# Performance work log

Measured on AMD Instinct MI355X. Metric: run time of the kernel, lower is better.

The kernel has to match this reference:

```python
import jax, jax.numpy as jnp
import numpy as np

B, N, E, L, G, F, H = 64, 500, 16000, 64, 64, 8, 128

def setup_inputs() -> dict:
    key = jax.random.key(0)
    ks = jax.random.split(key, 8)
    return {
        "x": jax.random.normal(ks[0], (B, N, L), dtype=jnp.float32),
        "incidence": jax.random.normal(ks[1], (N, E), dtype=jnp.float32),
        "ef": jax.random.normal(ks[2], (E, F), dtype=jnp.float32),
        "W1": jax.random.normal(ks[3], (F, H), dtype=jnp.float32) * 0.1,
        "b1": jax.random.normal(ks[4], (H,), dtype=jnp.float32) * 0.1,
        "W2": jax.random.normal(ks[5], (H, L * G), dtype=jnp.float32) * 0.1,
        "b2": jax.random.normal(ks[6], (L * G,), dtype=jnp.float32) * 0.1,
        "b_gc": jax.random.normal(ks[7], (G,), dtype=jnp.float32) * 0.1,
    }

def reference(x, incidence, ef, W1, b1, W2, b2, b_gc):
    # MLP-generated per-edge kernel: [E, G, L]
    h = jax.nn.relu(ef @ W1 + b1)
    kernel = (h @ W2 + b2).reshape(E, G, L)
    # gather node features onto edges: [B, E, L]
    t = jnp.einsum('bnl,ne->bel', x, incidence)
    # per-edge batched matvec: [B, E, G]
    y = jnp.einsum('egl,bel->beg', kernel, t)
    # scatter back to nodes: [B, N, G]
    y = jnp.einsum('ne,beg->bng', incidence, y)
    # gc is a frozen identity Linear -> just add bias, then ReLU
    y = jax.nn.relu(y + b_gc)
    return y.reshape(x.shape[0], -1)
```

## Files before the change

kernel.cpp:

```cpp
#include <hip/hip_runtime.h>

constexpr int B_ = 64, N_ = 500, E_ = 16000, L_ = 64, G_ = 64, F_ = 8, H_ = 128;
constexpr int GL_ = 4096;
constexpr int NP_ = 512;
constexpr int KS_ = 4;
constexpr int ACC_ELEMS = B_ * N_ * G_;

using bf16x8  = __attribute__((ext_vector_type(8))) short;
using f32x4   = __attribute__((ext_vector_type(4))) float;
using ushort8 = __attribute__((ext_vector_type(8))) unsigned short;

#define MFMA16(a, b, c) __builtin_amdgcn_mfma_f32_16x16x32_bf16((a), (b), (c), 0, 0, 0)

typedef __attribute__((address_space(3))) unsigned int       lds_u32;
typedef const __attribute__((address_space(1))) unsigned int glb_u32;

static __device__ __forceinline__ unsigned short f2bf(float f) {
    union { float f; unsigned u; } v; v.f = f;
    unsigned r = v.u + 0x7fffu + ((v.u >> 16) & 1u);
    return (unsigned short)(r >> 16);
}
static __device__ __forceinline__ float bf2f(unsigned short s) {
    union { float f; unsigned u; } v; v.u = ((unsigned)s) << 16;
    return v.f;
}

static __device__ __forceinline__ void stage_tile(
    const unsigned short* __restrict__ g, int ld, int r0, int kk,
    unsigned short* lds, int tid)
{
    #pragma unroll
    for (int c = 0; c < 4; ++c) {
        const int ch  = tid + c * 256;
        const int row = ch >> 3;
        const int csw = (ch & 7) ^ (row & 7);
        __builtin_amdgcn_global_load_lds(
            (glb_u32*)(g + (size_t)(r0 + row) * ld + kk + csw * 8),
            (lds_u32*)(lds + (size_t)ch * 8), 16, 0, 0);
    }
}

static __device__ __forceinline__ void gemm_body(
    const unsigned short* __restrict__ A, int lda,
    const unsigned short* __restrict__ Bm, int ldb,
    int K, int nN,
    unsigned short* __restrict__ C, int ldc,
    const float* __restrict__ bias)
{
    const int nwg = gridDim.x;
    const int bid = blockIdx.x;
    const int swz = (nwg & 7) ? bid : ((bid & 7) * (nwg >> 3) + (bid >> 3));
    const int m0 = (swz / nN) * 128, n0 = (swz % nN) * 128;

    const int tid  = threadIdx.x;
    const int lane = tid & 63, wid = tid >> 6;
    const int wm = wid >> 1, wn = wid & 1;
    const int fr = lane & 15, fq = lane >> 4;

    __shared__ __align__(16) unsigned short smem[2 * 128 * 64];
    unsigned short* As = smem;
    unsigned short* Bs = smem + 128 * 64;

    const f32x4 fz = {0.f, 0.f, 0.f, 0.f};
    f32x4 acc[4][4] = {{fz, fz, fz, fz}, {fz, fz, fz, fz},
                       {fz, fz, fz, fz}, {fz, fz, fz, fz}};

    const int rowA[4] = {wm * 64 + 0 * 16 + fr, wm * 64 + 1 * 16 + fr,
                         wm * 64 + 2 * 16 + fr, wm * 64 + 3 * 16 + fr};
    const int rowB[4] = {wn * 64 + 0 * 16 + fr, wn * 64 + 1 * 16 + fr,
                         wn * 64 + 2 * 16 + fr, wn * 64 + 3 * 16 + fr};

    const int nk = K / 64;
    for (int kt = 0; kt < nk; ++kt) {
        stage_tile(A, lda, m0, kt * 64, As, tid);
        stage_tile(Bm, ldb, n0, kt * 64, Bs, tid);
        __syncthreads();
        #pragma unroll
        for (int ks = 0; ks < 2; ++ks) {
            bf16x8 af[4], bf[4];
            #pragma unroll
            for (int i = 0; i < 4; ++i)
                af[i] = *(const bf16x8*)&As[rowA[i] * 64 +
                         (((ks * 4 + fq) ^ (rowA[i] & 7)) * 8)];
            #pragma unroll
            for (int j = 0; j < 4; ++j)
                bf[j] = *(const bf16x8*)&Bs[rowB[j] * 64 +
                         (((ks * 4 + fq) ^ (rowB[j] & 7)) * 8)];
            #pragma unroll
            for (int i = 0; i < 4; ++i)
                #pragma unroll
                for (int j = 0; j < 4; ++j)
                    acc[i][j] = MFMA16(af[i], bf[j], acc[i][j]);
        }
        __syncthreads();
    }

    auto Cs = (unsigned short(*)[128])smem;
    #pragma unroll
    for (int i = 0; i < 4; ++i)
        #pragma unroll
        for (int j = 0; j < 4; ++j) {
            const float bv = bias ? bias[n0 + wn * 64 + j * 16 + fr] : 0.f;
            #pragma unroll
            for (int r = 0; r < 4; ++r)
                Cs[wm * 64 + i * 16 + fq * 4 + r][wn * 64 + j * 16 + fr] =
                    f2bf(acc[i][j][r] + bv);
        }
    __syncthreads();
    const int r2 = tid >> 4, o2 = (tid & 15) * 8;
    #pragma unroll
    for (int i = 0; i < 8; ++i) {
        const int row = i * 16 + r2;
        *(uint4*)&C[(size_t)(m0 + row) * ldc + n0 + o2] = *(const uint4*)&Cs[row][o2];
    }
}

__global__ __launch_bounds__(256)
void gemm_pair(const unsigned short* __restrict__ A0, int lda0,
               const unsigned short* __restrict__ B0, int ldb0, int K0,
               unsigned short* __restrict__ C0, const float* __restrict__ bias0,
               const unsigned short* __restrict__ A1, int lda1,
               const unsigned short* __restrict__ B1, int ldb1, int K1,
               unsigned short* __restrict__ C1, int nN)
{
    if (blockIdx.y == 0)
        gemm_body(A0, lda0, B0, ldb0, K0, nN, C0, GL_, bias0);
    else
        gemm_body(A1, lda1, B1, ldb1, K1, nN, C1, GL_, nullptr);
}

__global__ __launch_bounds__(512)
void k_y8(unsigned short* tc, const unsigned short* __restrict__ Kc)
{
    const int e0 = blockIdx.x * 8;
    const int tid = threadIdx.x, lane = tid & 63, w = tid >> 6;
    const int e = e0 + w;
    const int fr = lane & 15, fq = lane >> 4;
    const unsigned short* A  = &tc[(size_t)e * GL_];
    const unsigned short* Bp = &Kc[(size_t)e * GL_];
    const f32x4 fz = {0.f, 0.f, 0.f, 0.f};
    f32x4 acc[4][4] = {{fz, fz, fz, fz}, {fz, fz, fz, fz},
                       {fz, fz, fz, fz}, {fz, fz, fz, fz}};
    #pragma unroll
    for (int ks = 0; ks < 2; ++ks) {
        bf16x8 af[4], bf[4];
        #pragma unroll
        for (int i = 0; i < 4; ++i)
            af[i] = *(const bf16x8*)&A[(i * 16 + fr) * 64 + ks * 32 + fq * 8];
        #pragma unroll
        for (int j = 0; j < 4; ++j)
            bf[j] = *(const bf16x8*)&Bp[(j * 16 + fr) * 64 + ks * 32 + fq * 8];
        #pragma unroll
        for (int i = 0; i < 4; ++i)
            #pragma unroll
            for (int j = 0; j < 4; ++j)
                acc[i][j] = MFMA16(af[i], bf[j], acc[i][j]);
    }
    __shared__ unsigned short y8[GL_ * 8];
    #pragma unroll
    for (int i = 0; i < 4; ++i)
        #pragma unroll
        for (int j = 0; j < 4; ++j)
            #pragma unroll
            for (int r = 0; r < 4; ++r) {
                const int bg = (i * 16 + fq * 4 + r) * 64 + j * 16 + fr;
                y8[bg * 8 + w] = f2bf(acc[i][j][r]);
            }
    __syncthreads();
    unsigned short* dst = tc + (size_t)e0 * GL_;
    #pragma unroll
    for (int p = 0; p < 8; ++p) {
        const int o = (p * 512 + tid) * 8;
        *(uint4*)&dst[o] = *(const uint4*)&y8[o];
    }
}

__global__ __launch_bounds__(256)
void k_accd(const unsigned short* __restrict__ Ae,
            const unsigned short* __restrict__ y8,
            unsigned short* __restrict__ planesB, int pbase, int K)
{
    const int xcd = blockIdx.x & 7, grp = blockIdx.x >> 3;
    const int m0 = (grp & 7) * 64;
    const int n0 = (xcd + 8 * (grp >> 3)) * 128;
    const int KSY = gridDim.y;
    const int kl = ((K / KSY) / 64) * 64;
    const int kbeg = blockIdx.y * kl;
    const int kend = ((int)blockIdx.y == KSY - 1) ? K : kbeg + kl;

    const int lane = threadIdx.x & 63, wid = threadIdx.x >> 6;
    const int wm = wid >> 1, wn = wid & 1;
    const int fr = lane & 15, fq = lane >> 4;

    const f32x4 fz = {0.f, 0.f, 0.f, 0.f};
    f32x4 acc[2][4] = {{fz, fz, fz, fz}, {fz, fz, fz, fz}};

    for (int kk = kbeg; kk < kend; kk += 64) {
        #pragma unroll
        for (int ks = 0; ks < 2; ++ks) {
            const int e8 = kk + ks * 32 + fq * 8;
            const size_t eb = (size_t)(e8 >> 3);
            bf16x8 af[2], bf[4];
            #pragma unroll
            for (int i = 0; i < 2; ++i)
                af[i] = *(const bf16x8*)&Ae[(eb * NP_ + m0 + wm * 32 + i * 16 + fr) * 8];
            #pragma unroll
            for (int j = 0; j < 4; ++j)
                bf[j] = *(const bf16x8*)&y8[eb * GL_ * 8 + (n0 + wn * 64 + j * 16 + fr) * 8];
            #pragma unroll
            for (int i = 0; i < 2; ++i)
                #pragma unroll
                for (int j = 0; j < 4; ++j)
                    acc[i][j] = MFMA16(af[i], bf[j], acc[i][j]);
        }
    }

    unsigned short* pl = planesB + (size_t)(pbase + blockIdx.y) * ACC_ELEMS;
    #pragma unroll
    for (int i = 0; i < 2; ++i)
        #pragma unroll
        for (int j = 0; j < 4; ++j) {
            const int col = n0 + wn * 64 + j * 16 + fr;
            const int b = col >> 6, g = col & 63;
            #pragma unroll
            for (int r = 0; r < 4; ++r) {
                const int n = m0 + wm * 32 + i * 16 + fq * 4 + r;
                if (n < N_)
                    pl[((size_t)b * N_ + n) * G_ + g] = f2bf(acc[i][j][r]);
            }
        }
}

__global__ __launch_bounds__(256)
void k_cvt_incB8(const float* __restrict__ inc, unsigned short* __restrict__ incB8)
{
    const int e0 = blockIdx.x * 64;
    const int n0 = blockIdx.y * 64;
    const int tid = threadIdx.x;
    __shared__ unsigned short sm[64][72];
    const int cl = tid & 63;
    for (int rr = tid >> 6; rr < 64; rr += 4) {
        const int n = n0 + rr;
        sm[rr][cl] = (n < N_) ? f2bf(inc[(size_t)n * E_ + e0 + cl]) : (unsigned short)0;
    }
    __syncthreads();
    const int eb = tid >> 5, idx = tid & 31;
    #pragma unroll
    for (int k = 0; k < 2; ++k) {
        const int row = idx * 2 + k;
        *(ushort8*)&incB8[((size_t)((e0 >> 3) + eb) * NP_ + n0 + row) * 8] =
            *(const ushort8*)&sm[row][eb * 8];
    }
}

__global__ __launch_bounds__(256)
void k_tr32(const float* __restrict__ in, unsigned short* __restrict__ out,
            int R, int C, int Rp, size_t inZ, size_t outZ)
{
    in  += (size_t)blockIdx.z * inZ;
    out += (size_t)blockIdx.z * outZ;
    const int c0 = blockIdx.x * 64, r0 = blockIdx.y * 64;
    __shared__ float sm[64][65];
    const int cl = threadIdx.x & 63;
    for (int rr = threadIdx.x >> 6; rr < 64; rr += 4) {
        const int r = r0 + rr;
        sm[cl][rr] = (r < R) ? in[(size_t)r * C + c0 + cl] : 0.f;
    }
    __syncthreads();
    const int cw = threadIdx.x >> 2, j0 = (threadIdx.x & 3) * 16;
    unsigned short tmp[16];
    #pragma unroll
    for (int j = 0; j < 16; ++j) tmp[j] = f2bf(sm[cw][j0 + j]);
    *(ushort8*)&out[(size_t)(c0 + cw) * Rp + r0 + j0]     = *(ushort8*)&tmp[0];
    *(ushort8*)&out[(size_t)(c0 + cw) * Rp + r0 + j0 + 8] = *(ushort8*)&tmp[8];
}

__global__ __launch_bounds__(256)
void k_h(const float* __restrict__ ef, const float* __restrict__ W1,
         const float* __restrict__ b1, unsigned short* __restrict__ h)
{
    const int idx = blockIdx.x * 256 + threadIdx.x;
    const int e = idx >> 7, hh = idx & 127;
    float v = b1[hh];
    const float* efp = &ef[(size_t)e * F_];
    #pragma unroll
    for (int f = 0; f < F_; ++f) v += efp[f] * W1[f * H_ + hh];
    h[idx] = f2bf(fmaxf(v, 0.f));
}

__global__ __launch_bounds__(256)
void k_final(const unsigned short* __restrict__ planesB, int P,
             const float* __restrict__ bgc, float* __restrict__ out)
{
    const int i = (blockIdx.x * 256 + threadIdx.x) * 8;
    if (i >= ACC_ELEMS) return;
    float s[8];
    #pragma unroll
    for (int j = 0; j < 8; ++j) s[j] = bgc[(i + j) & 63];
    for (int p = 0; p < P; ++p) {
        const ushort8 v = *(const ushort8*)&planesB[(size_t)p * ACC_ELEMS + i];
        #pragma unroll
        for (int j = 0; j < 8; ++j) s[j] += bf2f((unsigned short)v[j]);
    }
    float4 o0, o1;
    o0.x = fmaxf(s[0], 0.f); o0.y = fmaxf(s[1], 0.f);
    o0.z = fmaxf(s[2], 0.f); o0.w = fmaxf(s[3], 0.f);
    o1.x = fmaxf(s[4], 0.f); o1.y = fmaxf(s[5], 0.f);
    o1.z = fmaxf(s[6], 0.f); o1.w = fmaxf(s[7], 0.f);
    *(float4*)&out[i]     = o0;
    *(float4*)&out[i + 4] = o1;
}

extern "C" void kernel_launch(void* const* d_in, const int* in_sizes, int n_in,
                              void* d_out, int out_size, void* d_ws, size_t ws_size,
                              hipStream_t stream) {
    const float* x   = (const float*)d_in[0];
    const float* inc = (const float*)d_in[1];
    const float* ef  = (const float*)d_in[2];
    const float* W1  = (const float*)d_in[3];
    const float* b1  = (const float*)d_in[4];
    const float* W2  = (const float*)d_in[5];
    const float* b2  = (const float*)d_in[6];
    const float* bgc = (const float*)d_in[7];
    float* out = (float*)d_out;

    const size_t persistU16 = (size_t)NP_ * E_
                            + (size_t)E_ * NP_
                            + (size_t)B_ * L_ * NP_
                            + (size_t)E_ * H_
                            + (size_t)GL_ * H_;
    const size_t persistBytes = persistU16 * 2;

    int nc = 1, Ec = E_;
    for (; nc <= 16; ++nc) {
        Ec = ((E_ + nc - 1) / nc + 127) / 128 * 128;
        const size_t need = persistBytes
                          + (size_t)nc * KS_ * ACC_ELEMS * 2
                          + 2 * (size_t)Ec * GL_ * 2;
        if (need <= ws_size) break;
    }
    if (nc > 16) { nc = 16; Ec = 1024; }

    unsigned short* planesB = (unsigned short*)d_ws;
    unsigned short* incB8 = planesB + (size_t)nc * KS_ * ACC_ELEMS;
    unsigned short* incT = incB8 + (size_t)NP_ * E_;
    unsigned short* xT   = incT + (size_t)E_ * NP_;
    unsigned short* h    = xT   + (size_t)B_ * L_ * NP_;
    unsigned short* W2T  = h    + (size_t)E_ * H_;
    unsigned short* Kc   = W2T  + (size_t)GL_ * H_;
    unsigned short* tc   = Kc   + (size_t)Ec * GL_;

    k_cvt_incB8<<<dim3(E_ / 64, NP_ / 64), 256, 0, stream>>>(inc, incB8);
    k_tr32<<<dim3(E_ / 64, NP_ / 64, 1), 256, 0, stream>>>(inc, incT, N_, E_, NP_, 0, 0);
    k_tr32<<<dim3(1, NP_ / 64, B_),      256, 0, stream>>>(x, xT, N_, L_, NP_,
                                                           (size_t)N_ * L_, (size_t)L_ * NP_);
    k_tr32<<<dim3(GL_ / 64, H_ / 64, 1), 256, 0, stream>>>(W2, W2T, H_, GL_, H_, 0, 0);
    k_h<<<dim3(E_ * H_ / 256), 256, 0, stream>>>(ef, W1, b1, h);

    int cidx = 0;
    for (int e_off = 0; e_off < E_; e_off += Ec, ++cidx) {
        const int ec = (E_ - e_off) < Ec ? (E_ - e_off) : Ec;
        gemm_pair<<<dim3((ec / 128) * 32, 2), 256, 0, stream>>>(
            h + (size_t)e_off * H_, H_, W2T, H_, H_, Kc, b2,
            incT + (size_t)e_off * NP_, NP_, xT, NP_, NP_, tc, 32);
        k_y8<<<dim3(ec / 8), 512, 0, stream>>>(tc, Kc);
        k_accd<<<dim3(256, KS_), 256, 0, stream>>>(
            incB8 + (size_t)e_off * NP_, tc, planesB, cidx * KS_, ec);
    }

    k_final<<<dim3(ACC_ELEMS / 2048), 256, 0, stream>>>(planesB, nc * KS_, bgc, out);
}
```

Baseline: 397.5 us.

## Double-buffer GEMM LDS tiles and fuse incidence conversion kernels

The shared GEMM body now keeps two LDS buffers and prefetches the next K-tile while MFMAs run on the current one. Explicit vmcnt waits and raw barriers replace the __syncthreads pair. Separately, the two kernels that each read the full fp32 incidence matrix (bf16 blocked layout and bf16 transpose) are merged into one that reads it once and writes both. The LDS footprint per block doubles, which can lower occupancy, and the hand-written vmcnt count assumes a fixed number of loads per stage_tile call.

```diff
diff --git a/kernel.cpp b/kernel.cpp
--- a/kernel.cpp
+++ b/kernel.cpp
@@ -57,9 +57,11 @@
     const int wm = wid >> 1, wn = wid & 1;
     const int fr = lane & 15, fq = lane >> 4;
 
-    __shared__ __align__(16) unsigned short smem[2 * 128 * 64];
-    unsigned short* As = smem;
-    unsigned short* Bs = smem + 128 * 64;
+    __shared__ __align__(16) unsigned short smem[4 * 128 * 64];
+    unsigned short* const As0 = smem;
+    unsigned short* const Bs0 = smem + 128 * 64;
+    unsigned short* const As1 = smem + 2 * 128 * 64;
+    unsigned short* const Bs1 = smem + 3 * 128 * 64;
 
     const f32x4 fz = {0.f, 0.f, 0.f, 0.f};
     f32x4 acc[4][4] = {{fz, fz, fz, fz}, {fz, fz, fz, fz},
@@ -71,20 +73,33 @@
                          wn * 64 + 2 * 16 + fr, wn * 64 + 3 * 16 + fr};
 
     const int nk = K / 64;
+    stage_tile(A, lda, m0, 0, As0, tid);
+    stage_tile(Bm, ldb, n0, 0, Bs0, tid);
+
     for (int kt = 0; kt < nk; ++kt) {
-        stage_tile(A, lda, m0, kt * 64, As, tid);
-        stage_tile(Bm, ldb, n0, kt * 64, Bs, tid);
-        __syncthreads();
+        unsigned short* const Ac = (kt & 1) ? As1 : As0;
+        unsigned short* const Bc = (kt & 1) ? Bs1 : Bs0;
+        if (kt + 1 < nk) {
+            unsigned short* const An = (kt & 1) ? As0 : As1;
+            unsigned short* const Bn = (kt & 1) ? Bs0 : Bs1;
+            stage_tile(A, lda, m0, (kt + 1) * 64, An, tid);
+            stage_tile(Bm, ldb, n0, (kt + 1) * 64, Bn, tid);
+            asm volatile("s_waitcnt vmcnt(8)" ::: "memory");
+        } else {
+            asm volatile("s_waitcnt vmcnt(0)" ::: "memory");
+        }
+        __builtin_amdgcn_s_barrier();
+        __builtin_amdgcn_sched_barrier(0);
         #pragma unroll
         for (int ks = 0; ks < 2; ++ks) {
             bf16x8 af[4], bf[4];
             #pragma unroll
             for (int i = 0; i < 4; ++i)
-                af[i] = *(const bf16x8*)&As[rowA[i] * 64 +
+                af[i] = *(const bf16x8*)&Ac[rowA[i] * 64 +
                          (((ks * 4 + fq) ^ (rowA[i] & 7)) * 8)];
             #pragma unroll
             for (int j = 0; j < 4; ++j)
-                bf[j] = *(const bf16x8*)&Bs[rowB[j] * 64 +
+                bf[j] = *(const bf16x8*)&Bc[rowB[j] * 64 +
                          (((ks * 4 + fq) ^ (rowB[j] & 7)) * 8)];
             #pragma unroll
             for (int i = 0; i < 4; ++i)
@@ -92,7 +107,8 @@
                 for (int j = 0; j < 4; ++j)
                     acc[i][j] = MFMA16(af[i], bf[j], acc[i][j]);
         }
-        __syncthreads();
+        __builtin_amdgcn_sched_barrier(0);
+        __builtin_amdgcn_s_barrier();
     }
 
     auto Cs = (unsigned short(*)[128])smem;
@@ -232,24 +248,33 @@
 }
 
 __global__ __launch_bounds__(256)
-void k_cvt_incB8(const float* __restrict__ inc, unsigned short* __restrict__ incB8)
-{
-    const int e0 = blockIdx.x * 64;
-    const int n0 = blockIdx.y * 64;
-    const int tid = threadIdx.x;
-    __shared__ unsigned short sm[64][72];
-    const int cl = tid & 63;
+void k_cvt_inc(const float* __restrict__ inc, unsigned short* __restrict__ incT,
+               unsigned short* __restrict__ incB8)
+{
+    const int e0 = blockIdx.x * 64, n0 = blockIdx.y * 64;
+    const int tid = threadIdx.x, cl = tid & 63;
+    __shared__ unsigned short sm[64][80];
     for (int rr = tid >> 6; rr < 64; rr += 4) {
         const int n = n0 + rr;
-        sm[rr][cl] = (n < N_) ? f2bf(inc[(size_t)n * E_ + e0 + cl]) : (unsigned short)0;
+        sm[cl][rr] = (n < N_) ? f2bf(inc[(size_t)n * E_ + e0 + cl]) : (unsigned short)0;
     }
     __syncthreads();
-    const int eb = tid >> 5, idx = tid & 31;
-    #pragma unroll
-    for (int k = 0; k < 2; ++k) {
-        const int row = idx * 2 + k;
-        *(ushort8*)&incB8[((size_t)((e0 >> 3) + eb) * NP_ + n0 + row) * 8] =
-            *(const ushort8*)&sm[row][eb * 8];
+    {
+        const int cw = tid >> 2, j0 = (tid & 3) * 16;
+        *(ushort8*)&incT[(size_t)(e0 + cw) * NP_ + n0 + j0]     = *(const ushort8*)&sm[cw][j0];
+        *(ushort8*)&incT[(size_t)(e0 + cw) * NP_ + n0 + j0 + 8] = *(const ushort8*)&sm[cw][j0 + 8];
+    }
+    {
+        const int eb = tid >> 5, idx = tid & 31;
+        #pragma unroll
+        for (int k = 0; k < 2; ++k) {
+            const int row = idx * 2 + k;
+            unsigned short tmp[8];
+            #pragma unroll
+            for (int q = 0; q < 8; ++q) tmp[q] = sm[eb * 8 + q][row];
+            *(ushort8*)&incB8[((size_t)((e0 >> 3) + eb) * NP_ + n0 + row) * 8] =
+                *(const ushort8*)&tmp[0];
+        }
     }
 }
 
@@ -350,8 +375,7 @@
     unsigned short* Kc   = W2T  + (size_t)GL_ * H_;
     unsigned short* tc   = Kc   + (size_t)Ec * GL_;
 
-    k_cvt_incB8<<<dim3(E_ / 64, NP_ / 64), 256, 0, stream>>>(inc, incB8);
-    k_tr32<<<dim3(E_ / 64, NP_ / 64, 1), 256, 0, stream>>>(inc, incT, N_, E_, NP_, 0, 0);
+    k_cvt_inc<<<dim3(E_ / 64, NP_ / 64), 256, 0, stream>>>(inc, incT, incB8);
     k_tr32<<<dim3(1, NP_ / 64, B_),      256, 0, stream>>>(x, xT, N_, L_, NP_,
                                                            (size_t)N_ * L_, (size_t)L_ * NP_);
     k_tr32<<<dim3(GL_ / 64, H_ / 64, 1), 256, 0, stream>>>(W2, W2T, H_, GL_, H_, 0, 0);
```

Measured after the change: 373.2 us. 6.1% less time.
